# Performance work log

Hardware: AMD Instinct MI355X
Metric: run time of the kernel (lower is better)

The kernel has to match this reference:

```python
import jax, jax.numpy as jnp
import numpy as np

DIM, HEADS, PAIR_DIM = 256, 8, 128
B, S, N = 1, 128, 256
DH = DIM // HEADS
SCALE = DH ** -0.5
EPS = 1e-5


def setup_inputs() -> dict:
    key = jax.random.key(0)
    ks = jax.random.split(key, 12)
    s = lambda fan_in: 1.0 / np.sqrt(fan_in)
    return {
        "msa": jax.random.normal(ks[0], (B, S, N, DIM), jnp.float32),
        "pair": jax.random.normal(ks[1], (B, N, N, PAIR_DIM), jnp.float32),
        "mask": jax.random.randint(ks[2], (B, N, N), 0, 2, jnp.int32),
        "Wqkv": jax.random.normal(ks[3], (3 * DIM, DIM), jnp.float32) * s(DIM),
        "bqkv": jnp.zeros((3 * DIM,), jnp.float32),
        "Wout": jax.random.normal(ks[4], (DIM, DIM), jnp.float32) * s(DIM),
        "bout": jnp.zeros((DIM,), jnp.float32),
        "Wpb": jax.random.normal(ks[5], (HEADS, PAIR_DIM), jnp.float32) * s(PAIR_DIM),
        "bpb": jnp.zeros((HEADS,), jnp.float32),
        "gamma": jnp.ones((DIM,), jnp.float32),
        "beta": jnp.zeros((DIM,), jnp.float32),
    }


def reference(msa, pair, mask, Wqkv, bqkv, Wout, bout, Wpb, bpb, gamma, beta):
    # qkv projection: [B,S,N,3*DIM] -> [B,S,N,3,H,DH]
    qkv = (msa @ Wqkv.T + bqkv).reshape(B, S, N, 3, HEADS, DH)
    q, k, v = qkv[..., 0, :, :], qkv[..., 1, :, :], qkv[..., 2, :, :]
    # scores [B,S,H,N,N]
    attn = jnp.einsum('bsnhc,bsmhc->bshnm', q, k) * SCALE
    attn = jnp.where(mask[:, None, None, :, :] == 0, -1e9, attn)
    # pair bias: [B,N,N,P] -> [B,1,H,N,N]
    pair_bias = (pair @ Wpb.T + bpb).transpose(0, 3, 1, 2)[:, None]
    attn = jax.nn.softmax(attn + pair_bias, axis=-1)
    out = jnp.einsum('bshnm,bsmhc->bsnhc', attn, v).reshape(B, S, N, DIM)
    out = out @ Wout.T + bout
    # residual + layernorm
    x = msa + out
    mu = jnp.mean(x, axis=-1, keepdims=True)
    var = jnp.var(x, axis=-1, keepdims=True)
    return (x - mu) * jax.lax.rsqrt(var + EPS) * gamma + beta
```

## Files before the change

### kernel.cpp

```cpp
#include <hip/hip_runtime.h>
#include <cstdint>
#include <cstddef>

typedef unsigned short u16;
typedef __bf16 bf16x8 __attribute__((ext_vector_type(8)));
typedef float f32x4 __attribute__((ext_vector_type(4)));
typedef unsigned int u32x4 __attribute__((ext_vector_type(4)));

#define SCALE_QK 0.17677669529663687f

__device__ __forceinline__ u16 f2bf(float f){ return __builtin_bit_cast(u16, (__bf16)f); }
__device__ __forceinline__ bf16x8 ldfrag_g(const u16* p){
  return __builtin_bit_cast(bf16x8, *reinterpret_cast<const u32x4*>(p));
}

__global__ __launch_bounds__(256) void k_cvt(const float* __restrict__ src,
                                             u16* __restrict__ dst, int n4){
  int stride = gridDim.x * blockDim.x;
  for (int idx = blockIdx.x*blockDim.x + threadIdx.x; idx < n4; idx += stride){
    float4 v = reinterpret_cast<const float4*>(src)[idx];
    ushort4 o;
    o.x = f2bf(v.x); o.y = f2bf(v.y); o.z = f2bf(v.z); o.w = f2bf(v.w);
    reinterpret_cast<ushort4*>(dst)[idx] = o;
  }
}

__global__ __launch_bounds__(256) void k_pair_bias(const float* __restrict__ pair,
        const int* __restrict__ mask, const float* __restrict__ Wpb,
        const float* __restrict__ bpb, float* __restrict__ bias){
  __shared__ float wsm[8][128];
  __shared__ float bsm[8];
  int tid = threadIdx.x;
  for (int i = tid; i < 1024; i += 256) wsm[i>>7][i&127] = Wpb[i];
  if (tid < 8) bsm[tid] = bpb[tid];
  __syncthreads();
  int g = tid>>4, l = tid&15;
  int row = blockIdx.x*16 + g;
  const float4* p = reinterpret_cast<const float4*>(pair + (size_t)row*128);
  float4 a0 = p[l];
  float4 a1 = p[l+16];
  int c0 = 4*l, c1 = 64 + 4*l;
  float acc[8];
#pragma unroll
  for (int hh=0; hh<8; hh++){
    acc[hh] = a0.x*wsm[hh][c0] + a0.y*wsm[hh][c0+1] + a0.z*wsm[hh][c0+2] + a0.w*wsm[hh][c0+3]
            + a1.x*wsm[hh][c1] + a1.y*wsm[hh][c1+1] + a1.z*wsm[hh][c1+2] + a1.w*wsm[hh][c1+3];
  }
#pragma unroll
  for (int hh=0; hh<8; hh++){
    float v = acc[hh];
    v += __shfl_xor(v,1); v += __shfl_xor(v,2); v += __shfl_xor(v,4); v += __shfl_xor(v,8);
    acc[hh] = v;
  }
  if (l == 0){
    float mb = (mask[row] == 0) ? -1e9f : 0.0f;
#pragma unroll
    for (int hh=0; hh<8; hh++)
      bias[hh*65536 + row] = acc[hh] + bsm[hh] + mb;
  }
}

__global__ __launch_bounds__(256) void k_qkv(const u16* __restrict__ A,
                                             const u16* __restrict__ B,
                                             const float* __restrict__ bq,
                                             u16* __restrict__ qkv){
  __shared__ __align__(16) u16 Al[128*64];
  __shared__ __align__(16) u16 Bl[128*64];
  const int tid = threadIdx.x;
  const int w = tid>>6, l = tid&63;
  const int wm = w>>1, wn = w&1;
  const int m0 = blockIdx.y*128, n0 = blockIdx.x*128;
  const int lr = l&15, lg = l>>4;
  f32x4 acc[4][4] = {};
  for (int kt=0; kt<4; ++kt){
    const int k0 = kt*64;
    __syncthreads();
#pragma unroll
    for (int i=0;i<4;i++){
      int flat = tid + 256*i;
      int r = flat>>3, sl = flat&7;
      u32x4 da = *reinterpret_cast<const u32x4*>(A + (size_t)(m0+r)*256 + k0 + sl*8);
      u32x4 db = *reinterpret_cast<const u32x4*>(B + (size_t)(n0+r)*256 + k0 + sl*8);
      *reinterpret_cast<u32x4*>(&Al[r*64 + ((sl^(r&7))*8)]) = da;
      *reinterpret_cast<u32x4*>(&Bl[r*64 + ((sl^(r&7))*8)]) = db;
    }
    __syncthreads();
#pragma unroll
    for (int ks=0; ks<2; ++ks){
      bf16x8 af[4], bfr[4];
#pragma unroll
      for (int t=0;t<4;t++){
        int ra = wm*64 + t*16 + lr;
        int sa = (ks*4 + lg) ^ (ra&7);
        af[t] = __builtin_bit_cast(bf16x8, *reinterpret_cast<const u32x4*>(&Al[ra*64 + sa*8]));
        int rb = wn*64 + t*16 + lr;
        int sb = (ks*4 + lg) ^ (rb&7);
        bfr[t] = __builtin_bit_cast(bf16x8, *reinterpret_cast<const u32x4*>(&Bl[rb*64 + sb*8]));
      }
#pragma unroll
      for (int tm=0;tm<4;tm++)
#pragma unroll
        for (int tn=0;tn<4;tn++)
          acc[tm][tn] = __builtin_amdgcn_mfma_f32_16x16x32_bf16(af[tm], bfr[tn], acc[tm][tn], 0,0,0);
    }
  }
#pragma unroll
  for (int tn=0;tn<4;tn++){
    int c = n0 + wn*64 + tn*16 + lr;
    int t3 = c>>8, hh = (c>>5)&7, dh = c&31;
    float bb = bq[c];
    u16* obase = qkv + (size_t)(t3*8+hh)*32768*32 + dh;
#pragma unroll
    for (int tm=0;tm<4;tm++){
#pragma unroll
      for (int rr=0;rr<4;rr++){
        int m = m0 + wm*64 + tm*16 + lg*4 + rr;
        obase[(size_t)m*32] = f2bf(acc[tm][tn][rr] + bb);
      }
    }
  }
}

__global__ __launch_bounds__(256) void k_attn(const u16* __restrict__ qkv,
                                              const float* __restrict__ bias,
                                              u16* __restrict__ O){
  __shared__ __align__(16) u16 vT[32*256];
  __shared__ __align__(16) u16 P[4][64*64];
  const int h = blockIdx.x, s = blockIdx.y;
  const int tid = threadIdx.x;
  const int w = tid>>6, l = tid&63;
  const int lr = l&15, lg = l>>4;
  const u16* qb = qkv + ((size_t)(0*8+h)*32768 + s*256)*32;
  const u16* kb = qkv + ((size_t)(8+h)*32768 + s*256)*32;
  const u16* vb = qkv + ((size_t)(16+h)*32768 + s*256)*32;
  const float* bb = bias + h*65536;

#pragma unroll
  for (int i=0;i<4;i++){
    int flat4 = tid + 256*i;
    int m = flat4>>2, d0 = (flat4&3)*8;
    u32x4 d = *reinterpret_cast<const u32x4*>(vb + (size_t)m*32 + d0);
    u16 tmp[8];
    *reinterpret_cast<u32x4*>(tmp) = d;
#pragma unroll
    for (int j=0;j<8;j++){
      int dh = d0 + j;
      vT[dh*256 + (((m>>3)^(dh&7))*8) + (m&7)] = tmp[j];
    }
  }
  __syncthreads();

  bf16x8 qf[4];
#pragma unroll
  for (int tm=0;tm<4;tm++)
    qf[tm] = ldfrag_g(qb + (size_t)(64*w + tm*16 + lr)*32 + lg*8);

  f32x4 oacc[4][2] = {};
  float mrun[4][4], lrun[4][4];
#pragma unroll
  for (int tm=0;tm<4;tm++)
#pragma unroll
    for (int rr=0;rr<4;rr++){ mrun[tm][rr] = -3e38f; lrun[tm][rr] = 0.f; }

  for (int mt=0; mt<4; ++mt){
    bf16x8 kf[4];
#pragma unroll
    for (int tn=0;tn<4;tn++)
      kf[tn] = ldfrag_g(kb + (size_t)(mt*64 + tn*16 + lr)*32 + lg*8);
    f32x4 sacc[4][4] = {};
#pragma unroll
    for (int tm=0;tm<4;tm++)
#pragma unroll
      for (int tn=0;tn<4;tn++)
        sacc[tm][tn] = __builtin_amdgcn_mfma_f32_16x16x32_bf16(qf[tm], kf[tn], sacc[tm][tn], 0,0,0);
#pragma unroll
    for (int tm=0;tm<4;tm++){
#pragma unroll
      for (int rr=0;rr<4;rr++){
        int n = 64*w + tm*16 + lg*4 + rr;
        const float* brow = bb + n*256 + mt*64;
#pragma unroll
        for (int tn=0;tn<4;tn++)
          sacc[tm][tn][rr] = sacc[tm][tn][rr]*SCALE_QK + brow[tn*16 + lr];
      }
    }
#pragma unroll
    for (int tm=0;tm<4;tm++){
#pragma unroll
      for (int rr=0;rr<4;rr++){
        float mx = fmaxf(fmaxf(sacc[tm][0][rr], sacc[tm][1][rr]),
                         fmaxf(sacc[tm][2][rr], sacc[tm][3][rr]));
        mx = fmaxf(mx, __shfl_xor(mx,1));
        mx = fmaxf(mx, __shfl_xor(mx,2));
        mx = fmaxf(mx, __shfl_xor(mx,4));
        mx = fmaxf(mx, __shfl_xor(mx,8));
        float mo = mrun[tm][rr];
        float mn = fmaxf(mo, mx);
        float corr = __expf(mo - mn);
        mrun[tm][rr] = mn;
        float ps = 0.f;
#pragma unroll
        for (int tn=0;tn<4;tn++){
          float p = __expf(sacc[tm][tn][rr] - mn);
          sacc[tm][tn][rr] = p;
          ps += p;
        }
        ps += __shfl_xor(ps,1);
        ps += __shfl_xor(ps,2);
        ps += __shfl_xor(ps,4);
        ps += __shfl_xor(ps,8);
        lrun[tm][rr] = lrun[tm][rr]*corr + ps;
        oacc[tm][0][rr] *= corr;
        oacc[tm][1][rr] *= corr;
      }
    }
#pragma unroll
    for (int tm=0;tm<4;tm++){
#pragma unroll
      for (int rr=0;rr<4;rr++){
        int row = tm*16 + lg*4 + rr;
        int rb = row*64;
        int sx = row&7;
#pragma unroll
        for (int tn=0;tn<4;tn++){
          int col = tn*16 + lr;
          P[w][rb + (((col>>3)^sx)*8) + (col&7)] = f2bf(sacc[tm][tn][rr]);
        }
      }
    }
#pragma unroll
    for (int kk=0;kk<2;kk++){
      bf16x8 vf[2];
#pragma unroll
      for (int dt=0;dt<2;dt++){
        int c = dt*16 + lr;
        int slot = (mt*8 + kk*4 + lg) ^ (c&7);
        vf[dt] = __builtin_bit_cast(bf16x8, *reinterpret_cast<const u32x4*>(&vT[c*256 + slot*8]));
      }
#pragma unroll
      for (int tm=0;tm<4;tm++){
        int ra = tm*16 + lr;
        int sa = (kk*4 + lg) ^ (ra&7);
        bf16x8 pf = __builtin_bit_cast(bf16x8, *reinterpret_cast<const u32x4*>(&P[w][ra*64 + sa*8]));
        oacc[tm][0] = __builtin_amdgcn_mfma_f32_16x16x32_bf16(pf, vf[0], oacc[tm][0], 0,0,0);
        oacc[tm][1] = __builtin_amdgcn_mfma_f32_16x16x32_bf16(pf, vf[1], oacc[tm][1], 0,0,0);
      }
    }
  }
#pragma unroll
  for (int tm=0;tm<4;tm++){
#pragma unroll
    for (int rr=0;rr<4;rr++){
      int n = 64*w + tm*16 + lg*4 + rr;
      float inv = 1.0f / lrun[tm][rr];
      size_t rowb = (size_t)(s*256 + n)*256 + h*32;
#pragma unroll
      for (int dt=0;dt<2;dt++)
        O[rowb + dt*16 + lr] = f2bf(oacc[tm][dt][rr]*inv);
    }
  }
}

__global__ __launch_bounds__(256) void k_out_ln(const u16* __restrict__ A,
        const u16* __restrict__ Wo, const float* __restrict__ bo,
        const float* __restrict__ msa, const float* __restrict__ gamma,
        const float* __restrict__ beta, float* __restrict__ out){
  __shared__ __align__(16) u16 Al[64*64];
  __shared__ float redS[64][4];
  __shared__ float redQ[64][4];
  const int tid = threadIdx.x;
  const int w = tid>>6, l = tid&63;
  const int lr = l&15, lg = l>>4;
  const int m0 = blockIdx.x*64;
  f32x4 acc[4][4] = {};
  for (int kt=0;kt<4;kt++){
    const int k0 = kt*64;
    __syncthreads();
#pragma unroll
    for (int i=0;i<2;i++){
      int flat = tid + 256*i;
      int r = flat>>3, sl = flat&7;
      u32x4 d = *reinterpret_cast<const u32x4*>(A + (size_t)(m0+r)*256 + k0 + sl*8);
      *reinterpret_cast<u32x4*>(&Al[r*64 + ((sl^(r&7))*8)]) = d;
    }
    __syncthreads();
#pragma unroll
    for (int ks=0;ks<2;ks++){
      bf16x8 af[4], bfr[4];
#pragma unroll
      for (int t=0;t<4;t++){
        int ra = t*16 + lr;
        int sa = (ks*4+lg) ^ (ra&7);
        af[t] = __builtin_bit_cast(bf16x8, *reinterpret_cast<const u32x4*>(&Al[ra*64 + sa*8]));
        int c = w*64 + t*16 + lr;
        bfr[t] = ldfrag_g(Wo + (size_t)c*256 + k0 + ks*32 + lg*8);
      }
#pragma unroll
      for (int tm=0;tm<4;tm++)
#pragma unroll
        for (int tn=0;tn<4;tn++)
          acc[tm][tn] = __builtin_amdgcn_mfma_f32_16x16x32_bf16(af[tm], bfr[tn], acc[tm][tn], 0,0,0);
    }
  }
#pragma unroll
  for (int tn=0;tn<4;tn++){
    int c = w*64 + tn*16 + lr;
    float bc = bo[c];
#pragma unroll
    for (int tm=0;tm<4;tm++)
#pragma unroll
      for (int rr=0;rr<4;rr++){
        int m = m0 + tm*16 + lg*4 + rr;
        acc[tm][tn][rr] += bc + msa[(size_t)m*256 + c];
      }
  }
#pragma unroll
  for (int tm=0;tm<4;tm++){
#pragma unroll
    for (int rr=0;rr<4;rr++){
      float sS = 0.f, sQ = 0.f;
#pragma unroll
      for (int tn=0;tn<4;tn++){
        float v = acc[tm][tn][rr];
        sS += v; sQ += v*v;
      }
      sS += __shfl_xor(sS,1); sS += __shfl_xor(sS,2); sS += __shfl_xor(sS,4); sS += __shfl_xor(sS,8);
      sQ += __shfl_xor(sQ,1); sQ += __shfl_xor(sQ,2); sQ += __shfl_xor(sQ,4); sQ += __shfl_xor(sQ,8);
      if (lr == 0){
        int row = tm*16 + lg*4 + rr;
        redS[row][w] = sS;
        redQ[row][w] = sQ;
      }
    }
  }
  __syncthreads();
#pragma unroll
  for (int tm=0;tm<4;tm++){
#pragma unroll
    for (int rr=0;rr<4;rr++){
      int row = tm*16 + lg*4 + rr;
      float S = redS[row][0]+redS[row][1]+redS[row][2]+redS[row][3];
      float Q = redQ[row][0]+redQ[row][1]+redQ[row][2]+redQ[row][3];
      float mu = S * (1.0f/256.0f);
      float var = Q * (1.0f/256.0f) - mu*mu;
      float inv = rsqrtf(var + 1e-5f);
      int m = m0 + row;
#pragma unroll
      for (int tn=0;tn<4;tn++){
        int c = w*64 + tn*16 + lr;
        out[(size_t)m*256 + c] = (acc[tm][tn][rr]-mu)*inv*gamma[c] + beta[c];
      }
    }
  }
}

extern "C" void kernel_launch(void* const* d_in, const int* in_sizes, int n_in,
                              void* d_out, int out_size, void* d_ws, size_t ws_size,
                              hipStream_t stream) {
  const float* msa  = (const float*)d_in[0];
  const float* pair = (const float*)d_in[1];
  const int*   mask = (const int*)d_in[2];
  const float* Wqkv = (const float*)d_in[3];
  const float* bqkv = (const float*)d_in[4];
  const float* Wout = (const float*)d_in[5];
  const float* bout = (const float*)d_in[6];
  const float* Wpb  = (const float*)d_in[7];
  const float* bpb  = (const float*)d_in[8];
  const float* gamma= (const float*)d_in[9];
  const float* beta = (const float*)d_in[10];
  float* out = (float*)d_out;

  char* ws = (char*)d_ws;
  u16*   msa_bf  = (u16*)(ws);
  u16*   wqkv_bf = (u16*)(ws + 16777216);
  u16*   wout_bf = (u16*)(ws + 17170432);
  float* biasb   = (float*)(ws + 17301504);
  u16*   qkvb    = (u16*)(ws + 19398656);
  u16*   Ob      = (u16*)(ws + 69730304);

  k_cvt<<<4096, 256, 0, stream>>>(msa,  msa_bf,  8388608/4);
  k_cvt<<<192,  256, 0, stream>>>(Wqkv, wqkv_bf, 196608/4);
  k_cvt<<<64,   256, 0, stream>>>(Wout, wout_bf, 65536/4);
  k_pair_bias<<<4096, 256, 0, stream>>>(pair, mask, Wpb, bpb, biasb);
  k_qkv<<<dim3(6,256), 256, 0, stream>>>(msa_bf, wqkv_bf, bqkv, qkvb);
  k_attn<<<dim3(8,128), 256, 0, stream>>>(qkvb, biasb, Ob);
  k_out_ln<<<512, 256, 0, stream>>>(Ob, wout_bf, bout, msa, gamma, beta, out);
}
```

Baseline: 259.8 us.

## Use bf16 transposed pair bias, split attention rows, direct-to-LDS loads in GEMMs

```diff
diff --git a/kernel.cpp b/kernel.cpp
--- a/kernel.cpp
+++ b/kernel.cpp
@@ -10,8 +10,13 @@
 #define SCALE_QK 0.17677669529663687f
 
 __device__ __forceinline__ u16 f2bf(float f){ return __builtin_bit_cast(u16, (__bf16)f); }
+__device__ __forceinline__ float bf2f(u16 u){ unsigned v = ((unsigned)u)<<16; return __builtin_bit_cast(float, v); }
 __device__ __forceinline__ bf16x8 ldfrag_g(const u16* p){
   return __builtin_bit_cast(bf16x8, *reinterpret_cast<const u32x4*>(p));
+}
+__device__ __forceinline__ void gload16(const u16* g, u16* lds){
+  __builtin_amdgcn_global_load_lds((const __attribute__((address_space(1))) unsigned int*)g,
+                                   (__attribute__((address_space(3))) unsigned int*)lds, 16, 0, 0);
 }
 
 __global__ __launch_bounds__(256) void k_cvt(const float* __restrict__ src,
@@ -25,9 +30,25 @@
   }
 }
 
+__global__ __launch_bounds__(256) void k_cvt2(const float* __restrict__ a, u16* __restrict__ da,
+                                              const float* __restrict__ b, u16* __restrict__ db){
+  int bid = blockIdx.x;
+  if (bid < 192){
+    int idx = bid*256 + threadIdx.x;
+    float4 v = reinterpret_cast<const float4*>(a)[idx];
+    ushort4 o; o.x=f2bf(v.x); o.y=f2bf(v.y); o.z=f2bf(v.z); o.w=f2bf(v.w);
+    reinterpret_cast<ushort4*>(da)[idx] = o;
+  } else {
+    int idx = (bid-192)*256 + threadIdx.x;
+    float4 v = reinterpret_cast<const float4*>(b)[idx];
+    ushort4 o; o.x=f2bf(v.x); o.y=f2bf(v.y); o.z=f2bf(v.z); o.w=f2bf(v.w);
+    reinterpret_cast<ushort4*>(db)[idx] = o;
+  }
+}
+
 __global__ __launch_bounds__(256) void k_pair_bias(const float* __restrict__ pair,
         const int* __restrict__ mask, const float* __restrict__ Wpb,
-        const float* __restrict__ bpb, float* __restrict__ bias){
+        const float* __restrict__ bpb, u16* __restrict__ bT){
   __shared__ float wsm[8][128];
   __shared__ float bsm[8];
   int tid = threadIdx.x;
@@ -54,16 +75,17 @@
   }
   if (l == 0){
     float mb = (mask[row] == 0) ? -1e9f : 0.0f;
+    int n = row>>8, m = row&255;
 #pragma unroll
     for (int hh=0; hh<8; hh++)
-      bias[hh*65536 + row] = acc[hh] + bsm[hh] + mb;
-  }
-}
-
-__global__ __launch_bounds__(256) void k_qkv(const u16* __restrict__ A,
-                                             const u16* __restrict__ B,
-                                             const float* __restrict__ bq,
-                                             u16* __restrict__ qkv){
+      bT[hh*65536 + m*256 + n] = f2bf(acc[hh] + bsm[hh] + mb);
+  }
+}
+
+__global__ __launch_bounds__(256, 3) void k_qkv(const u16* __restrict__ A,
+                                                const u16* __restrict__ B,
+                                                const float* __restrict__ bq,
+                                                u16* __restrict__ qkv){
   __shared__ __align__(16) u16 Al[128*64];
   __shared__ __align__(16) u16 Bl[128*64];
   const int tid = threadIdx.x;
@@ -76,13 +98,11 @@
     const int k0 = kt*64;
     __syncthreads();
 #pragma unroll
-    for (int i=0;i<4;i++){
-      int flat = tid + 256*i;
-      int r = flat>>3, sl = flat&7;
-      u32x4 da = *reinterpret_cast<const u32x4*>(A + (size_t)(m0+r)*256 + k0 + sl*8);
-      u32x4 db = *reinterpret_cast<const u32x4*>(B + (size_t)(n0+r)*256 + k0 + sl*8);
-      *reinterpret_cast<u32x4*>(&Al[r*64 + ((sl^(r&7))*8)]) = da;
-      *reinterpret_cast<u32x4*>(&Bl[r*64 + ((sl^(r&7))*8)]) = db;
+    for (int j=0;j<4;j++){
+      int ch = w*256 + j*64 + l;
+      int r = ch>>3, sl = ch&7;
+      gload16(A + (size_t)(m0+r)*256 + k0 + ((sl^(r&7))*8), Al + (size_t)(w*256 + j*64)*8);
+      gload16(B + (size_t)(n0+r)*256 + k0 + ((sl^(r&7))*8), Bl + (size_t)(w*256 + j*64)*8);
     }
     __syncthreads();
 #pragma unroll
@@ -121,19 +141,20 @@
   }
 }
 
-__global__ __launch_bounds__(256) void k_attn(const u16* __restrict__ qkv,
-                                              const float* __restrict__ bias,
-                                              u16* __restrict__ O){
+__global__ __launch_bounds__(256, 3) void k_attn(const u16* __restrict__ qkv,
+                                                 const u16* __restrict__ bT,
+                                                 u16* __restrict__ O){
   __shared__ __align__(16) u16 vT[32*256];
-  __shared__ __align__(16) u16 P[4][64*64];
-  const int h = blockIdx.x, s = blockIdx.y;
+  __shared__ __align__(16) u16 P[4][32*64];
+  const int h = blockIdx.x, s = blockIdx.y, z = blockIdx.z;
   const int tid = threadIdx.x;
   const int w = tid>>6, l = tid&63;
   const int lr = l&15, lg = l>>4;
-  const u16* qb = qkv + ((size_t)(0*8+h)*32768 + s*256)*32;
+  const int n0 = z*128 + 32*w;
+  const u16* qb = qkv + ((size_t)h*32768 + s*256)*32;
   const u16* kb = qkv + ((size_t)(8+h)*32768 + s*256)*32;
   const u16* vb = qkv + ((size_t)(16+h)*32768 + s*256)*32;
-  const float* bb = bias + h*65536;
+  const u16* bb = bT + h*65536;
 
 #pragma unroll
   for (int i=0;i<4;i++){
@@ -150,81 +171,86 @@
   }
   __syncthreads();
 
-  bf16x8 qf[4];
-#pragma unroll
-  for (int tm=0;tm<4;tm++)
-    qf[tm] = ldfrag_g(qb + (size_t)(64*w + tm*16 + lr)*32 + lg*8);
-
-  f32x4 oacc[4][2] = {};
-  float mrun[4][4], lrun[4][4];
-#pragma unroll
-  for (int tm=0;tm<4;tm++)
-#pragma unroll
-    for (int rr=0;rr<4;rr++){ mrun[tm][rr] = -3e38f; lrun[tm][rr] = 0.f; }
+  bf16x8 qf[2];
+#pragma unroll
+  for (int t=0;t<2;t++)
+    qf[t] = ldfrag_g(qb + (size_t)(n0 + t*16 + lr)*32 + lg*8);
+
+  f32x4 oacc[2][2] = {};
+  float mrun[2][4], lrun[2][4];
+#pragma unroll
+  for (int t=0;t<2;t++)
+#pragma unroll
+    for (int rr=0;rr<4;rr++){ mrun[t][rr] = -3e38f; lrun[t][rr] = 0.f; }
 
   for (int mt=0; mt<4; ++mt){
+    ushort4 b4[2][4];
+#pragma unroll
+    for (int t=0;t<2;t++)
+#pragma unroll
+      for (int tn=0;tn<4;tn++)
+        b4[t][tn] = *reinterpret_cast<const ushort4*>(
+            bb + (size_t)(mt*64 + tn*16 + lr)*256 + n0 + t*16 + lg*4);
     bf16x8 kf[4];
 #pragma unroll
     for (int tn=0;tn<4;tn++)
       kf[tn] = ldfrag_g(kb + (size_t)(mt*64 + tn*16 + lr)*32 + lg*8);
-    f32x4 sacc[4][4] = {};
-#pragma unroll
-    for (int tm=0;tm<4;tm++)
+    f32x4 sacc[2][4] = {};
+#pragma unroll
+    for (int t=0;t<2;t++)
 #pragma unroll
       for (int tn=0;tn<4;tn++)
-        sacc[tm][tn] = __builtin_amdgcn_mfma_f32_16x16x32_bf16(qf[tm], kf[tn], sacc[tm][tn], 0,0,0);
-#pragma unroll
-    for (int tm=0;tm<4;tm++){
+        sacc[t][tn] = __builtin_amdgcn_mfma_f32_16x16x32_bf16(qf[t], kf[tn], sacc[t][tn], 0,0,0);
+#pragma unroll
+    for (int t=0;t<2;t++)
+#pragma unroll
+      for (int tn=0;tn<4;tn++){
+        float bc[4] = { bf2f(b4[t][tn].x), bf2f(b4[t][tn].y), bf2f(b4[t][tn].z), bf2f(b4[t][tn].w) };
+#pragma unroll
+        for (int rr=0;rr<4;rr++)
+          sacc[t][tn][rr] = sacc[t][tn][rr]*SCALE_QK + bc[rr];
+      }
+#pragma unroll
+    for (int t=0;t<2;t++){
 #pragma unroll
       for (int rr=0;rr<4;rr++){
-        int n = 64*w + tm*16 + lg*4 + rr;
-        const float* brow = bb + n*256 + mt*64;
-#pragma unroll
-        for (int tn=0;tn<4;tn++)
-          sacc[tm][tn][rr] = sacc[tm][tn][rr]*SCALE_QK + brow[tn*16 + lr];
-      }
-    }
-#pragma unroll
-    for (int tm=0;tm<4;tm++){
-#pragma unroll
-      for (int rr=0;rr<4;rr++){
-        float mx = fmaxf(fmaxf(sacc[tm][0][rr], sacc[tm][1][rr]),
-                         fmaxf(sacc[tm][2][rr], sacc[tm][3][rr]));
+        float mx = fmaxf(fmaxf(sacc[t][0][rr], sacc[t][1][rr]),
+                         fmaxf(sacc[t][2][rr], sacc[t][3][rr]));
         mx = fmaxf(mx, __shfl_xor(mx,1));
         mx = fmaxf(mx, __shfl_xor(mx,2));
         mx = fmaxf(mx, __shfl_xor(mx,4));
         mx = fmaxf(mx, __shfl_xor(mx,8));
-        float mo = mrun[tm][rr];
+        float mo = mrun[t][rr];
         float mn = fmaxf(mo, mx);
         float corr = __expf(mo - mn);
-        mrun[tm][rr] = mn;
+        mrun[t][rr] = mn;
         float ps = 0.f;
 #pragma unroll
         for (int tn=0;tn<4;tn++){
-          float p = __expf(sacc[tm][tn][rr] - mn);
-          sacc[tm][tn][rr] = p;
+          float p = __expf(sacc[t][tn][rr] - mn);
+          sacc[t][tn][rr] = p;
           ps += p;
         }
         ps += __shfl_xor(ps,1);
         ps += __shfl_xor(ps,2);
         ps += __shfl_xor(ps,4);
         ps += __shfl_xor(ps,8);
-        lrun[tm][rr] = lrun[tm][rr]*corr + ps;
-        oacc[tm][0][rr] *= corr;
-        oacc[tm][1][rr] *= corr;
-      }
-    }
-#pragma unroll
-    for (int tm=0;tm<4;tm++){
+        lrun[t][rr] = lrun[t][rr]*corr + ps;
+        oacc[t][0][rr] *= corr;
+        oacc[t][1][rr] *= corr;
+      }
+    }
+#pragma unroll
+    for (int t=0;t<2;t++){
 #pragma unroll
       for (int rr=0;rr<4;rr++){
-        int row = tm*16 + lg*4 + rr;
+        int row = t*16 + lg*4 + rr;
         int rb = row*64;
         int sx = row&7;
 #pragma unroll
         for (int tn=0;tn<4;tn++){
           int col = tn*16 + lr;
-          P[w][rb + (((col>>3)^sx)*8) + (col&7)] = f2bf(sacc[tm][tn][rr]);
+          P[w][rb + (((col>>3)^sx)*8) + (col&7)] = f2bf(sacc[t][tn][rr]);
         }
       }
     }
@@ -238,34 +264,35 @@
         vf[dt] = __builtin_bit_cast(bf16x8, *reinterpret_cast<const u32x4*>(&vT[c*256 + slot*8]));
       }
 #pragma unroll
-      for (int tm=0;tm<4;tm++){
-        int ra = tm*16 + lr;
+      for (int t=0;t<2;t++){
+        int ra = t*16 + lr;
         int sa = (kk*4 + lg) ^ (ra&7);
         bf16x8 pf = __builtin_bit_cast(bf16x8, *reinterpret_cast<const u32x4*>(&P[w][ra*64 + sa*8]));
-        oacc[tm][0] = __builtin_amdgcn_mfma_f32_16x16x32_bf16(pf, vf[0], oacc[tm][0], 0,0,0);
-        oacc[tm][1] = __builtin_amdgcn_mfma_f32_16x16x32_bf16(pf, vf[1], oacc[tm][1], 0,0,0);
-      }
-    }
-  }
-#pragma unroll
-  for (int tm=0;tm<4;tm++){
+        oacc[t][0] = __builtin_amdgcn_mfma_f32_16x16x32_bf16(pf, vf[0], oacc[t][0], 0,0,0);
+        oacc[t][1] = __builtin_amdgcn_mfma_f32_16x16x32_bf16(pf, vf[1], oacc[t][1], 0,0,0);
+      }
+    }
+  }
+#pragma unroll
+  for (int t=0;t<2;t++){
 #pragma unroll
     for (int rr=0;rr<4;rr++){
-      int n = 64*w + tm*16 + lg*4 + rr;
-      float inv = 1.0f / lrun[tm][rr];
+      int n = n0 + t*16 + lg*4 + rr;
+      float inv = 1.0f / lrun[t][rr];
       size_t rowb = (size_t)(s*256 + n)*256 + h*32;
 #pragma unroll
       for (int dt=0;dt<2;dt++)
-        O[rowb + dt*16 + lr] = f2bf(oacc[tm][dt][rr]*inv);
-    }
-  }
-}
-
-__global__ __launch_bounds__(256) void k_out_ln(const u16* __restrict__ A,
+        O[rowb + dt*16 + lr] = f2bf(oacc[t][dt][rr]*inv);
+    }
+  }
+}
+
+__global__ __launch_bounds__(256, 3) void k_out_ln(const u16* __restrict__ A,
         const u16* __restrict__ Wo, const float* __restrict__ bo,
         const float* __restrict__ msa, const float* __restrict__ gamma,
         const float* __restrict__ beta, float* __restrict__ out){
   __shared__ __align__(16) u16 Al[64*64];
+  __shared__ __align__(16) u16 Wl[256*64];
   __shared__ float redS[64][4];
   __shared__ float redQ[64][4];
   const int tid = threadIdx.x;
@@ -277,11 +304,16 @@
     const int k0 = kt*64;
     __syncthreads();
 #pragma unroll
-    for (int i=0;i<2;i++){
-      int flat = tid + 256*i;
-      int r = flat>>3, sl = flat&7;
-      u32x4 d = *reinterpret_cast<const u32x4*>(A + (size_t)(m0+r)*256 + k0 + sl*8);
-      *reinterpret_cast<u32x4*>(&Al[r*64 + ((sl^(r&7))*8)]) = d;
+    for (int j=0;j<2;j++){
+      int ch = w*128 + j*64 + l;
+      int r = ch>>3, sl = ch&7;
+      gload16(A + (size_t)(m0+r)*256 + k0 + ((sl^(r&7))*8), Al + (size_t)(w*128 + j*64)*8);
+    }
+#pragma unroll
+    for (int j=0;j<8;j++){
+      int ch = w*512 + j*64 + l;
+      int r = ch>>3, sl = ch&7;
+      gload16(Wo + (size_t)r*256 + k0 + ((sl^(r&7))*8), Wl + (size_t)(w*512 + j*64)*8);
     }
     __syncthreads();
 #pragma unroll
@@ -292,8 +324,9 @@
         int ra = t*16 + lr;
         int sa = (ks*4+lg) ^ (ra&7);
         af[t] = __builtin_bit_cast(bf16x8, *reinterpret_cast<const u32x4*>(&Al[ra*64 + sa*8]));
-        int c = w*64 + t*16 + lr;
-        bfr[t] = ldfrag_g(Wo + (size_t)c*256 + k0 + ks*32 + lg*8);
+        int rb = w*64 + t*16 + lr;
+        int sb = (ks*4+lg) ^ (rb&7);
+        bfr[t] = __builtin_bit_cast(bf16x8, *reinterpret_cast<const u32x4*>(&Wl[rb*64 + sb*8]));
       }
 #pragma unroll
       for (int tm=0;tm<4;tm++)
@@ -374,15 +407,14 @@
   u16*   msa_bf  = (u16*)(ws);
   u16*   wqkv_bf = (u16*)(ws + 16777216);
   u16*   wout_bf = (u16*)(ws + 17170432);
-  float* biasb   = (float*)(ws + 17301504);
-  u16*   qkvb    = (u16*)(ws + 19398656);
-  u16*   Ob      = (u16*)(ws + 69730304);
-
-  k_cvt<<<4096, 256, 0, stream>>>(msa,  msa_bf,  8388608/4);
-  k_cvt<<<192,  256, 0, stream>>>(Wqkv, wqkv_bf, 196608/4);
-  k_cvt<<<64,   256, 0, stream>>>(Wout, wout_bf, 65536/4);
-  k_pair_bias<<<4096, 256, 0, stream>>>(pair, mask, Wpb, bpb, biasb);
+  u16*   biasT   = (u16*)(ws + 17301504);
+  u16*   qkvb    = (u16*)(ws + 18350080);
+  u16*   Ob      = (u16*)(ws + 68681728);
+
+  k_cvt<<<4096, 256, 0, stream>>>(msa, msa_bf, 8388608/4);
+  k_cvt2<<<256, 256, 0, stream>>>(Wqkv, wqkv_bf, Wout, wout_bf);
+  k_pair_bias<<<4096, 256, 0, stream>>>(pair, mask, Wpb, bpb, biasT);
   k_qkv<<<dim3(6,256), 256, 0, stream>>>(msa_bf, wqkv_bf, bqkv, qkvb);
-  k_attn<<<dim3(8,128), 256, 0, stream>>>(qkvb, biasb, Ob);
+  k_attn<<<dim3(8,128,2), 256, 0, stream>>>(qkvb, biasT, Ob);
   k_out_ln<<<512, 256, 0, stream>>>(Ob, wout_bf, bout, msa, gamma, beta, out);
 }
```

Measured after the change: 248.2 us. -4.5%, faster.
